# Kernel tuning notes

Hardware: AMD Instinct MI355X
Metric: run time of the kernel (lower is better)

The kernel has to match this reference:

```python
import jax, jax.numpy as jnp
import numpy as np

B = 2048
HID = 256      # hidden_dim (latent)
COND = 128     # cond_dim
NCH = 64       # n_chars
MAXLEN = 128   # max_len
R = 256        # recurrent_dim


def setup_inputs() -> dict:
    key = jax.random.key(0)
    ks = jax.random.split(key, 10)
    s = 0.05
    return {
        "z": jax.random.normal(ks[0], (B, HID), jnp.float32),
        "x_cond": jax.random.normal(ks[1], (B, COND), jnp.float32),
        # latent_to_hidden: Linear(hidden_dim + cond_dim -> recurrent_dim)
        "W_lh": jax.random.normal(ks[2], (R, HID + COND), jnp.float32) * s,
        "b_lh": jax.random.normal(ks[3], (R,), jnp.float32) * s,
        # GRU (single layer): weights in PyTorch gate order [r, z, n]
        "W_ih": jax.random.normal(ks[4], (3 * R, R), jnp.float32) * s,
        "W_hh": jax.random.normal(ks[5], (3 * R, R), jnp.float32) * s,
        "b_ih": jax.random.normal(ks[6], (3 * R,), jnp.float32) * s,
        "b_hh": jax.random.normal(ks[7], (3 * R,), jnp.float32) * s,
        # output_layer: Linear(recurrent_dim -> n_chars)
        "W_out": jax.random.normal(ks[8], (NCH, R), jnp.float32) * s,
        "b_out": jax.random.normal(ks[9], (NCH,), jnp.float32) * s,
    }


def _gru_cell(x, h, W_ih, W_hh, b_ih, b_hh):
    # PyTorch GRU cell: gates ordered [reset, update, new]
    gi = x @ W_ih.T + b_ih          # (B, 3R)
    gh = h @ W_hh.T + b_hh          # (B, 3R)
    i_r, i_z, i_n = jnp.split(gi, 3, axis=-1)
    h_r, h_z, h_n = jnp.split(gh, 3, axis=-1)
    r = jax.nn.sigmoid(i_r + h_r)
    u = jax.nn.sigmoid(i_z + h_z)
    n = jnp.tanh(i_n + r * h_n)
    return (1.0 - u) * n + u * h


def reference(z, x_cond, W_lh, b_lh, W_ih, W_hh, b_ih, b_hh, W_out, b_out):
    # Generation branch (teacher_force_inputs is None), dropout=0.0
    zc = jnp.concatenate([z, x_cond], axis=1)          # (B, HID+COND)
    h0 = zc @ W_lh.T + b_lh                            # (B, R), gru_depth=1
    x0 = jnp.zeros((z.shape[0], R), dtype=z.dtype)     # initial input step

    def step(carry, _):
        h, xin = carry
        hn = _gru_cell(xin, h, W_ih, W_hh, b_ih, b_hh)  # (B, R)
        logits = hn @ W_out.T + b_out                   # (B, NCH)
        return (hn, hn), logits                         # next input = GRU output

    (_, _), ys = jax.lax.scan(step, (h0, x0), None, length=MAXLEN)
    return jnp.transpose(ys, (1, 0, 2))                 # (B, MAXLEN, NCH)
```

## Files before the change

### kernel.cpp

```cpp
#include <hip/hip_runtime.h>
#include <hip/hip_bf16.h>

#define BATCH 2048
#define HID 256
#define COND 128
#define NCH 64
#define MAXLEN 128
#define RDIM 256

#define WCAT_OFF 0
#define WHH0_OFF 262144
#define WLH_OFF  524288
#define WOUT_OFF 622592
#define BCAT_OFF 638976
#define BCAT0_OFF 640000

__global__ void prep_kernel(const float* __restrict__ W_lh,
                            const float* __restrict__ W_ih, const float* __restrict__ W_hh,
                            const float* __restrict__ b_ih, const float* __restrict__ b_hh,
                            const float* __restrict__ W_out, float* __restrict__ ws) {
    int gid = blockIdx.x * blockDim.x + threadIdx.x;
    if (gid < 384 * 256) {
        int k = gid >> 8, u = gid & 255;
        ws[WLH_OFF + gid] = W_lh[u * 384 + k];
    }
    if (gid < 65536) {
        int k = gid >> 8, u = gid & 255;
        float ir = W_ih[u * 256 + k], iz = W_ih[(256 + u) * 256 + k], inw = W_ih[(512 + u) * 256 + k];
        float hr = W_hh[u * 256 + k], hz = W_hh[(256 + u) * 256 + k], hnw = W_hh[(512 + u) * 256 + k];
        int base = WCAT_OFF + k * 1024 + u * 4;
        ws[base + 0] = ir + hr; ws[base + 1] = iz + hz; ws[base + 2] = inw; ws[base + 3] = hnw;
        base = WHH0_OFF + k * 1024 + u * 4;
        ws[base + 0] = hr; ws[base + 1] = hz; ws[base + 2] = hnw; ws[base + 3] = 0.0f;
    }
    if (gid < 16384) {
        int k = gid >> 6, o = gid & 63;
        ws[WOUT_OFF + k * 64 + o] = W_out[o * 256 + k];
    }
    if (gid < 256) {
        int u = gid;
        float bir = b_ih[u], biz = b_ih[256 + u];
        float bhr = b_hh[u], bhz = b_hh[256 + u], bhn = b_hh[512 + u];
        int base = BCAT_OFF + u * 4;
        ws[base + 0] = bir + bhr; ws[base + 1] = biz + bhz; ws[base + 2] = b_ih[512 + u]; ws[base + 3] = bhn;
        base = BCAT0_OFF + u * 4;
        ws[base + 0] = bir + bhr; ws[base + 1] = biz + bhz; ws[base + 2] = bhn; ws[base + 3] = 0.0f;
    }
}

__device__ __forceinline__ float sigm(float x)   { return 1.0f / (1.0f + __expf(-x)); }
__device__ __forceinline__ float tanh_f(float x) { return 1.0f - 2.0f / (1.0f + __expf(2.0f * x)); }

__global__ __launch_bounds__(256)
void gru_persist(const float* __restrict__ z, const float* __restrict__ xc,
                 const float* __restrict__ b_lh, const float* __restrict__ b_ih,
                 const float* __restrict__ b_out_g,
                 const float* __restrict__ ws, float* __restrict__ out) {
    __shared__ __align__(16) float lds_h[8 * 256];
    __shared__ __align__(16) float lds_w[256 * 64];

    const int t  = threadIdx.x;
    const int b0 = blockIdx.x * 8;

    for (int idx = t; idx < 8 * 384; idx += 256) {
        int i = idx / 384, k = idx - i * 384;
        float v = (k < 256) ? z[(b0 + i) * 256 + k] : xc[(b0 + i) * 128 + (k - 256)];
        lds_w[i * 384 + k] = v;
    }
    __syncthreads();

    float h_own[8];
    {
        float acc[8];
        float blh = b_lh[t];
#pragma unroll
        for (int i = 0; i < 8; i++) acc[i] = blh;
        const float* Wlh = ws + WLH_OFF;
        for (int k4 = 0; k4 < 96; ++k4) {
            int k = k4 * 4;
            float w0 = Wlh[(k + 0) * 256 + t];
            float w1 = Wlh[(k + 1) * 256 + t];
            float w2 = Wlh[(k + 2) * 256 + t];
            float w3 = Wlh[(k + 3) * 256 + t];
#pragma unroll
            for (int i = 0; i < 8; i++) {
                const float4 hv = *(const float4*)&lds_w[i * 384 + k];
                acc[i] += hv.x * w0 + hv.y * w1 + hv.z * w2 + hv.w * w3;
            }
        }
#pragma unroll
        for (int i = 0; i < 8; i++) { h_own[i] = acc[i]; lds_h[i * 256 + t] = acc[i]; }
    }
    __syncthreads();

    {
        const float* Wo = ws + WOUT_OFF;
        for (int idx = t; idx < 16384; idx += 256) lds_w[idx] = Wo[idx];
    }
    __syncthreads();

    const float4* Wcat = (const float4*)(ws + WCAT_OFF);
    const float4* Whh0 = (const float4*)(ws + WHH0_OFF);
    const float4 bc1 = ((const float4*)(ws + BCAT_OFF))[t];
    const float4 bc0 = ((const float4*)(ws + BCAT0_OFF))[t];
    const float bin_c = b_ih[512 + t];
    const int olane = t & 63, rg = t >> 6;
    const float bout = b_out_g[olane];
    float* outp = out + (long)b0 * MAXLEN * NCH;

    for (int st = 0; st < MAXLEN; ++st) {
        const float4* Wp = (st == 0) ? Whh0 : Wcat;
        const float4 bc = (st == 0) ? bc0 : bc1;
        float ax[8], ay[8], az[8], aw[8];
#pragma unroll
        for (int i = 0; i < 8; i++) { ax[i] = bc.x; ay[i] = bc.y; az[i] = bc.z; aw[i] = bc.w; }

#pragma unroll 2
        for (int k4 = 0; k4 < 64; ++k4) {
            int k = k4 * 4;
            float4 w0 = Wp[(k + 0) * 256 + t];
            float4 w1 = Wp[(k + 1) * 256 + t];
            float4 w2 = Wp[(k + 2) * 256 + t];
            float4 w3 = Wp[(k + 3) * 256 + t];
#pragma unroll
            for (int i = 0; i < 8; i++) {
                const float4 hv = *(const float4*)&lds_h[i * 256 + k];
                ax[i] += hv.x * w0.x; ay[i] += hv.x * w0.y; az[i] += hv.x * w0.z; aw[i] += hv.x * w0.w;
                ax[i] += hv.y * w1.x; ay[i] += hv.y * w1.y; az[i] += hv.y * w1.z; aw[i] += hv.y * w1.w;
                ax[i] += hv.z * w2.x; ay[i] += hv.z * w2.y; az[i] += hv.z * w2.z; aw[i] += hv.z * w2.w;
                ax[i] += hv.w * w3.x; ay[i] += hv.w * w3.y; az[i] += hv.w * w3.z; aw[i] += hv.w * w3.w;
            }
        }

        float hn_[8];
        if (st == 0) {
#pragma unroll
            for (int i = 0; i < 8; i++) {
                float r = sigm(ax[i]); float uu = sigm(ay[i]);
                float n = tanh_f(bin_c + r * az[i]);
                hn_[i] = (1.0f - uu) * n + uu * h_own[i];
            }
        } else {
#pragma unroll
            for (int i = 0; i < 8; i++) {
                float r = sigm(ax[i]); float uu = sigm(ay[i]);
                float n = tanh_f(az[i] + r * aw[i]);
                hn_[i] = (1.0f - uu) * n + uu * h_own[i];
            }
        }
        __syncthreads();
#pragma unroll
        for (int i = 0; i < 8; i++) { lds_h[i * 256 + t] = hn_[i]; h_own[i] = hn_[i]; }
        __syncthreads();

        {
            float l0 = bout, l1 = bout;
            const int r0 = 2 * rg, r1 = 2 * rg + 1;
            for (int k4 = 0; k4 < 64; ++k4) {
                int k = k4 * 4;
                const float4 h0v = *(const float4*)&lds_h[r0 * 256 + k];
                const float4 h1v = *(const float4*)&lds_h[r1 * 256 + k];
                float wq0 = lds_w[(k + 0) * 64 + olane];
                float wq1 = lds_w[(k + 1) * 64 + olane];
                float wq2 = lds_w[(k + 2) * 64 + olane];
                float wq3 = lds_w[(k + 3) * 64 + olane];
                l0 += h0v.x * wq0 + h0v.y * wq1 + h0v.z * wq2 + h0v.w * wq3;
                l1 += h1v.x * wq0 + h1v.y * wq1 + h1v.z * wq2 + h1v.w * wq3;
            }
            outp[(long)r0 * MAXLEN * NCH + st * NCH + olane] = l0;
            outp[(long)r1 * MAXLEN * NCH + st * NCH + olane] = l1;
        }
    }
}

extern "C" void kernel_launch(void* const* d_in, const int* in_sizes, int n_in,
                              void* d_out, int out_size, void* d_ws, size_t ws_size,
                              hipStream_t stream) {
    const float* z     = (const float*)d_in[0];
    const float* xcond = (const float*)d_in[1];
    const float* W_lh  = (const float*)d_in[2];
    const float* b_lh  = (const float*)d_in[3];
    const float* W_ih  = (const float*)d_in[4];
    const float* W_hh  = (const float*)d_in[5];
    const float* b_ih  = (const float*)d_in[6];
    const float* b_hh  = (const float*)d_in[7];
    const float* W_out = (const float*)d_in[8];
    const float* b_out = (const float*)d_in[9];
    float* out = (float*)d_out;
    float* ws  = (float*)d_ws;

    hipLaunchKernelGGL(prep_kernel, dim3(384), dim3(256), 0, stream,
                       W_lh, W_ih, W_hh, b_ih, b_hh, W_out, ws);
    hipLaunchKernelGGL(gru_persist, dim3(256), dim3(256), 0, stream,
                       z, xcond, b_lh, b_ih, b_out, ws, out);
}
```

Measured before the change: 3.634 ms.

## Split GRU K-reduction across four wavegroups and overlap output projection with next step

Grows each block from 256 to 1024 threads. The 256-wide recurrent reduction is split four ways by K, with partial sums combined through LDS, so each thread's serial FMA chain per step is a quarter as long. The output-logit projection for the previous step now runs on the upper threads during the next step's reduction and reads W_out directly from global memory, so the LDS weight copy and its transpose in the prep kernel are dropped. The costs are extra LDS traffic and barriers for the partial-sum reduction, nonlinearities serialized on one quarter of the threads, and the launch bound of 1024 threads with 4 waves per EU may limit registers.

New measurement: 3.873 ms. +6.6%, slower.

```diff
diff --git a/kernel.cpp b/kernel.cpp
--- a/kernel.cpp
+++ b/kernel.cpp
@@ -11,14 +11,13 @@
 #define WCAT_OFF 0
 #define WHH0_OFF 262144
 #define WLH_OFF  524288
-#define WOUT_OFF 622592
 #define BCAT_OFF 638976
 #define BCAT0_OFF 640000
 
 __global__ void prep_kernel(const float* __restrict__ W_lh,
                             const float* __restrict__ W_ih, const float* __restrict__ W_hh,
                             const float* __restrict__ b_ih, const float* __restrict__ b_hh,
-                            const float* __restrict__ W_out, float* __restrict__ ws) {
+                            float* __restrict__ ws) {
     int gid = blockIdx.x * blockDim.x + threadIdx.x;
     if (gid < 384 * 256) {
         int k = gid >> 8, u = gid & 255;
@@ -33,10 +32,6 @@
         base = WHH0_OFF + k * 1024 + u * 4;
         ws[base + 0] = hr; ws[base + 1] = hz; ws[base + 2] = hnw; ws[base + 3] = 0.0f;
     }
-    if (gid < 16384) {
-        int k = gid >> 6, o = gid & 63;
-        ws[WOUT_OFF + k * 64 + o] = W_out[o * 256 + k];
-    }
     if (gid < 256) {
         int u = gid;
         float bir = b_ih[u], biz = b_ih[256 + u];
@@ -51,77 +46,83 @@
 __device__ __forceinline__ float sigm(float x)   { return 1.0f / (1.0f + __expf(-x)); }
 __device__ __forceinline__ float tanh_f(float x) { return 1.0f - 2.0f / (1.0f + __expf(2.0f * x)); }
 
-__global__ __launch_bounds__(256)
+__global__ __launch_bounds__(1024, 4)
 void gru_persist(const float* __restrict__ z, const float* __restrict__ xc,
                  const float* __restrict__ b_lh, const float* __restrict__ b_ih,
-                 const float* __restrict__ b_out_g,
+                 const float* __restrict__ W_out, const float* __restrict__ b_out_g,
                  const float* __restrict__ ws, float* __restrict__ out) {
     __shared__ __align__(16) float lds_h[8 * 256];
-    __shared__ __align__(16) float lds_w[256 * 64];
-
-    const int t  = threadIdx.x;
-    const int b0 = blockIdx.x * 8;
-
-    for (int idx = t; idx < 8 * 384; idx += 256) {
+    __shared__ __align__(16) float4 bufv[3 * 8 * 256];
+
+    const int tid = threadIdx.x;
+    const int u   = tid & 255;
+    const int q   = tid >> 8;
+    const int b0  = blockIdx.x * 8;
+
+    float* zcs = (float*)bufv;
+    for (int idx = tid; idx < 8 * 384; idx += 1024) {
         int i = idx / 384, k = idx - i * 384;
-        float v = (k < 256) ? z[(b0 + i) * 256 + k] : xc[(b0 + i) * 128 + (k - 256)];
-        lds_w[i * 384 + k] = v;
+        zcs[idx] = (k < 256) ? z[(b0 + i) * 256 + k] : xc[(b0 + i) * 128 + (k - 256)];
     }
     __syncthreads();
 
     float h_own[8];
-    {
+    if (q == 0) {
         float acc[8];
-        float blh = b_lh[t];
+        float blh = b_lh[u];
 #pragma unroll
         for (int i = 0; i < 8; i++) acc[i] = blh;
         const float* Wlh = ws + WLH_OFF;
         for (int k4 = 0; k4 < 96; ++k4) {
             int k = k4 * 4;
-            float w0 = Wlh[(k + 0) * 256 + t];
-            float w1 = Wlh[(k + 1) * 256 + t];
-            float w2 = Wlh[(k + 2) * 256 + t];
-            float w3 = Wlh[(k + 3) * 256 + t];
+            float w0 = Wlh[(k + 0) * 256 + u];
+            float w1 = Wlh[(k + 1) * 256 + u];
+            float w2 = Wlh[(k + 2) * 256 + u];
+            float w3 = Wlh[(k + 3) * 256 + u];
 #pragma unroll
             for (int i = 0; i < 8; i++) {
-                const float4 hv = *(const float4*)&lds_w[i * 384 + k];
+                const float4 hv = *(const float4*)&zcs[i * 384 + k];
                 acc[i] += hv.x * w0 + hv.y * w1 + hv.z * w2 + hv.w * w3;
             }
         }
 #pragma unroll
-        for (int i = 0; i < 8; i++) { h_own[i] = acc[i]; lds_h[i * 256 + t] = acc[i]; }
-    }
-    __syncthreads();
-
-    {
-        const float* Wo = ws + WOUT_OFF;
-        for (int idx = t; idx < 16384; idx += 256) lds_w[idx] = Wo[idx];
+        for (int i = 0; i < 8; i++) { h_own[i] = acc[i]; lds_h[i * 256 + u] = acc[i]; }
     }
     __syncthreads();
 
     const float4* Wcat = (const float4*)(ws + WCAT_OFF);
     const float4* Whh0 = (const float4*)(ws + WHH0_OFF);
-    const float4 bc1 = ((const float4*)(ws + BCAT_OFF))[t];
-    const float4 bc0 = ((const float4*)(ws + BCAT0_OFF))[t];
-    const float bin_c = b_ih[512 + t];
-    const int olane = t & 63, rg = t >> 6;
-    const float bout = b_out_g[olane];
+    const float4  bc1  = ((const float4*)(ws + BCAT_OFF))[u];
+    const float4  bc0  = ((const float4*)(ws + BCAT0_OFF))[u];
+    const float   bin_c = b_ih[512 + u];
+    const int kbase = q * 64;
+
+    const int lo_o = tid & 63;
+    const int lo_r = (tid - 512) >> 6;
+    const float bout = (tid >= 512) ? b_out_g[lo_o] : 0.0f;
+    const float4* Woutv = (const float4*)(W_out);
+    const float4* ldshv = (const float4*)lds_h;
     float* outp = out + (long)b0 * MAXLEN * NCH;
 
     for (int st = 0; st < MAXLEN; ++st) {
         const float4* Wp = (st == 0) ? Whh0 : Wcat;
-        const float4 bc = (st == 0) ? bc0 : bc1;
         float ax[8], ay[8], az[8], aw[8];
-#pragma unroll
-        for (int i = 0; i < 8; i++) { ax[i] = bc.x; ay[i] = bc.y; az[i] = bc.z; aw[i] = bc.w; }
+        if (q == 0) {
+            const float4 bc = (st == 0) ? bc0 : bc1;
+#pragma unroll
+            for (int i = 0; i < 8; i++) { ax[i] = bc.x; ay[i] = bc.y; az[i] = bc.z; aw[i] = bc.w; }
+        } else {
+#pragma unroll
+            for (int i = 0; i < 8; i++) { ax[i] = 0.0f; ay[i] = 0.0f; az[i] = 0.0f; aw[i] = 0.0f; }
+        }
 
 #pragma unroll 2
-        for (int k4 = 0; k4 < 64; ++k4) {
-            int k = k4 * 4;
-            float4 w0 = Wp[(k + 0) * 256 + t];
-            float4 w1 = Wp[(k + 1) * 256 + t];
-            float4 w2 = Wp[(k + 2) * 256 + t];
-            float4 w3 = Wp[(k + 3) * 256 + t];
+        for (int k4 = 0; k4 < 16; ++k4) {
+            int k = kbase + k4 * 4;
+            float4 w0 = Wp[(k + 0) * 256 + u];
+            float4 w1 = Wp[(k + 1) * 256 + u];
+            float4 w2 = Wp[(k + 2) * 256 + u];
+            float4 w3 = Wp[(k + 3) * 256 + u];
 #pragma unroll
             for (int i = 0; i < 8; i++) {
                 const float4 hv = *(const float4*)&lds_h[i * 256 + k];
@@ -132,44 +133,64 @@
             }
         }
 
-        float hn_[8];
-        if (st == 0) {
-#pragma unroll
-            for (int i = 0; i < 8; i++) {
-                float r = sigm(ax[i]); float uu = sigm(ay[i]);
-                float n = tanh_f(bin_c + r * az[i]);
-                hn_[i] = (1.0f - uu) * n + uu * h_own[i];
-            }
-        } else {
-#pragma unroll
-            for (int i = 0; i < 8; i++) {
-                float r = sigm(ax[i]); float uu = sigm(ay[i]);
-                float n = tanh_f(az[i] + r * aw[i]);
-                hn_[i] = (1.0f - uu) * n + uu * h_own[i];
-            }
-        }
+        if (q) {
+#pragma unroll
+            for (int i = 0; i < 8; i++)
+                bufv[(q - 1) * 2048 + i * 256 + u] = make_float4(ax[i], ay[i], az[i], aw[i]);
+        }
+
+        if (tid >= 512 && st > 0) {
+            float l = bout;
+#pragma unroll 4
+            for (int k4 = 0; k4 < 64; ++k4) {
+                const float4 w = Woutv[lo_o * 64 + k4];
+                const float4 h = ldshv[lo_r * 64 + k4];
+                l += h.x * w.x + h.y * w.y + h.z * w.z + h.w * w.w;
+            }
+            outp[(long)lo_r * MAXLEN * NCH + (st - 1) * NCH + lo_o] = l;
+        }
+
         __syncthreads();
-#pragma unroll
-        for (int i = 0; i < 8; i++) { lds_h[i * 256 + t] = hn_[i]; h_own[i] = hn_[i]; }
+
+        if (q == 0) {
+#pragma unroll
+            for (int qq = 0; qq < 3; ++qq)
+#pragma unroll
+                for (int i = 0; i < 8; ++i) {
+                    const float4 p = bufv[qq * 2048 + i * 256 + u];
+                    ax[i] += p.x; ay[i] += p.y; az[i] += p.z; aw[i] += p.w;
+                }
+            float hn_[8];
+            if (st == 0) {
+#pragma unroll
+                for (int i = 0; i < 8; i++) {
+                    float r = sigm(ax[i]); float uu = sigm(ay[i]);
+                    float n = tanh_f(bin_c + r * az[i]);
+                    hn_[i] = (1.0f - uu) * n + uu * h_own[i];
+                }
+            } else {
+#pragma unroll
+                for (int i = 0; i < 8; i++) {
+                    float r = sigm(ax[i]); float uu = sigm(ay[i]);
+                    float n = tanh_f(az[i] + r * aw[i]);
+                    hn_[i] = (1.0f - uu) * n + uu * h_own[i];
+                }
+            }
+#pragma unroll
+            for (int i = 0; i < 8; i++) { lds_h[i * 256 + u] = hn_[i]; h_own[i] = hn_[i]; }
+        }
         __syncthreads();
-
-        {
-            float l0 = bout, l1 = bout;
-            const int r0 = 2 * rg, r1 = 2 * rg + 1;
-            for (int k4 = 0; k4 < 64; ++k4) {
-                int k = k4 * 4;
-                const float4 h0v = *(const float4*)&lds_h[r0 * 256 + k];
-                const float4 h1v = *(const float4*)&lds_h[r1 * 256 + k];
-                float wq0 = lds_w[(k + 0) * 64 + olane];
-                float wq1 = lds_w[(k + 1) * 64 + olane];
-                float wq2 = lds_w[(k + 2) * 64 + olane];
-                float wq3 = lds_w[(k + 3) * 64 + olane];
-                l0 += h0v.x * wq0 + h0v.y * wq1 + h0v.z * wq2 + h0v.w * wq3;
-                l1 += h1v.x * wq0 + h1v.y * wq1 + h1v.z * wq2 + h1v.w * wq3;
-            }
-            outp[(long)r0 * MAXLEN * NCH + st * NCH + olane] = l0;
-            outp[(long)r1 * MAXLEN * NCH + st * NCH + olane] = l1;
-        }
+    }
+
+    if (tid >= 512) {
+        float l = bout;
+#pragma unroll 4
+        for (int k4 = 0; k4 < 64; ++k4) {
+            const float4 w = Woutv[lo_o * 64 + k4];
+            const float4 h = ldshv[lo_r * 64 + k4];
+            l += h.x * w.x + h.y * w.y + h.z * w.z + h.w * w.w;
+        }
+        outp[(long)lo_r * MAXLEN * NCH + (MAXLEN - 1) * NCH + lo_o] = l;
     }
 }
 
@@ -190,7 +211,7 @@
     float* ws  = (float*)d_ws;
 
     hipLaunchKernelGGL(prep_kernel, dim3(384), dim3(256), 0, stream,
-                       W_lh, W_ih, W_hh, b_ih, b_hh, W_out, ws);
-    hipLaunchKernelGGL(gru_persist, dim3(256), dim3(256), 0, stream,
-                       z, xcond, b_lh, b_ih, b_out, ws, out);
+                       W_lh, W_ih, W_hh, b_ih, b_hh, ws);
+    hipLaunchKernelGGL(gru_persist, dim3(256), dim3(1024), 0, stream,
+                       z, xcond, b_lh, b_ih, W_out, b_out, ws, out);
 }
```

## Split GRU K-reduction across four wavegroups with LDS partial-sum exchange

Applied to the files above, without the earlier changes.

The block grows from 256 to 1024 threads: each quarter of threads computes a partial matvec over a 64-wide slice of the hidden dimension for all 8 rows, then writes the partials to LDS. Each thread then reduces the partials for two rows and applies the gate math. The output projection is deferred by one step, reads W_out from global memory instead of LDS, and is split in two halves reduced through LDS. The goal is more parallelism per CU on the serial recurrence. In exchange the kernel uses more LDS, adds a partial-sum exchange every step, and repeatedly streams W_out from global/L2.

Result: faster. 3.333 ms (-8.3%).

```diff
diff --git a/kernel.cpp b/kernel.cpp
--- a/kernel.cpp
+++ b/kernel.cpp
@@ -2,8 +2,6 @@
 #include <hip/hip_bf16.h>
 
 #define BATCH 2048
-#define HID 256
-#define COND 128
 #define NCH 64
 #define MAXLEN 128
 #define RDIM 256
@@ -34,7 +32,7 @@
         ws[base + 0] = hr; ws[base + 1] = hz; ws[base + 2] = hnw; ws[base + 3] = 0.0f;
     }
     if (gid < 16384) {
-        int k = gid >> 6, o = gid & 63;
+        int o = gid & 63, k = gid >> 6;
         ws[WOUT_OFF + k * 64 + o] = W_out[o * 256 + k];
     }
     if (gid < 256) {
@@ -51,125 +49,156 @@
 __device__ __forceinline__ float sigm(float x)   { return 1.0f / (1.0f + __expf(-x)); }
 __device__ __forceinline__ float tanh_f(float x) { return 1.0f - 2.0f / (1.0f + __expf(2.0f * x)); }
 
-__global__ __launch_bounds__(256)
+__global__ __launch_bounds__(1024, 1)
 void gru_persist(const float* __restrict__ z, const float* __restrict__ xc,
                  const float* __restrict__ b_lh, const float* __restrict__ b_ih,
                  const float* __restrict__ b_out_g,
                  const float* __restrict__ ws, float* __restrict__ out) {
     __shared__ __align__(16) float lds_h[8 * 256];
-    __shared__ __align__(16) float lds_w[256 * 64];
-
-    const int t  = threadIdx.x;
-    const int b0 = blockIdx.x * 8;
-
-    for (int idx = t; idx < 8 * 384; idx += 256) {
+    __shared__ __align__(16) float4 pbufv[4 * 6 * 256];
+    __shared__ float lbuf[1024];
+
+    const int tid = threadIdx.x;
+    const int u   = tid & 255;
+    const int q   = __builtin_amdgcn_readfirstlane(tid >> 8);
+    const int b0  = blockIdx.x * 8;
+
+    float* zcs = (float*)pbufv;
+    for (int idx = tid; idx < 8 * 384; idx += 1024) {
         int i = idx / 384, k = idx - i * 384;
-        float v = (k < 256) ? z[(b0 + i) * 256 + k] : xc[(b0 + i) * 128 + (k - 256)];
-        lds_w[i * 384 + k] = v;
+        zcs[idx] = (k < 256) ? z[(b0 + i) * 256 + k] : xc[(b0 + i) * 128 + (k - 256)];
     }
     __syncthreads();
 
-    float h_own[8];
+    float h_own0, h_own1;
     {
-        float acc[8];
-        float blh = b_lh[t];
-#pragma unroll
-        for (int i = 0; i < 8; i++) acc[i] = blh;
-        const float* Wlh = ws + WLH_OFF;
+        float a0 = b_lh[u], a1 = a0;
+        const float* Wlh = ws + WLH_OFF + u;
+        const float* zr0 = zcs + (2 * q) * 384;
+        const float* zr1 = zr0 + 384;
+#pragma unroll 2
         for (int k4 = 0; k4 < 96; ++k4) {
-            int k = k4 * 4;
-            float w0 = Wlh[(k + 0) * 256 + t];
-            float w1 = Wlh[(k + 1) * 256 + t];
-            float w2 = Wlh[(k + 2) * 256 + t];
-            float w3 = Wlh[(k + 3) * 256 + t];
-#pragma unroll
-            for (int i = 0; i < 8; i++) {
-                const float4 hv = *(const float4*)&lds_w[i * 384 + k];
-                acc[i] += hv.x * w0 + hv.y * w1 + hv.z * w2 + hv.w * w3;
+            int k = 4 * k4;
+            float w0 = Wlh[(k + 0) * 256];
+            float w1 = Wlh[(k + 1) * 256];
+            float w2 = Wlh[(k + 2) * 256];
+            float w3 = Wlh[(k + 3) * 256];
+            const float4 v0 = *(const float4*)(zr0 + k);
+            const float4 v1 = *(const float4*)(zr1 + k);
+            a0 += v0.x * w0 + v0.y * w1 + v0.z * w2 + v0.w * w3;
+            a1 += v1.x * w0 + v1.y * w1 + v1.z * w2 + v1.w * w3;
+        }
+        h_own0 = a0; h_own1 = a1;
+        lds_h[(2 * q) * 256 + u] = a0;
+        lds_h[(2 * q + 1) * 256 + u] = a1;
+    }
+    __syncthreads();
+
+    const float4* Wcat  = (const float4*)(ws + WCAT_OFF);
+    const float4* Whh0v = (const float4*)(ws + WHH0_OFF);
+    const float4  bc1   = ((const float4*)(ws + BCAT_OFF))[u];
+    const float4  bc0v  = ((const float4*)(ws + BCAT0_OFF))[u];
+    const float   bin_c = b_ih[512 + u];
+
+    int ro[8];
+#pragma unroll
+    for (int jj = 0; jj < 8; ++jj) ro[jj] = (((2 * q + jj) & 7) << 8);
+
+    const int lkh = tid & 1;
+    const float* hrow_base = lds_h + ((tid >> 1) >> 6) * 256 + lkh * 128;
+    const float* wcolT = ws + WOUT_OFF + lkh * 128 * 64 + ((tid >> 1) & 63);
+    const int co = tid & 63, cr = tid >> 6;
+    const float bout = b_out_g[co];
+    float* outp = out + (long)b0 * MAXLEN * NCH;
+
+    for (int st = 0; st < MAXLEN; ++st) {
+        const float4* Wp = st ? Wcat : Whh0v;
+        float ax[8], ay[8], az[8], aw[8];
+#pragma unroll
+        for (int jj = 0; jj < 8; ++jj) { ax[jj] = 0.f; ay[jj] = 0.f; az[jj] = 0.f; aw[jj] = 0.f; }
+
+        const float4* wbase = Wp + (q * 64) * 256 + u;
+        const float*  hbase = lds_h + q * 64;
+
+#pragma unroll 2
+        for (int k4 = 0; k4 < 16; ++k4) {
+            const float4 w0 = wbase[(4 * k4 + 0) * 256];
+            const float4 w1 = wbase[(4 * k4 + 1) * 256];
+            const float4 w2 = wbase[(4 * k4 + 2) * 256];
+            const float4 w3 = wbase[(4 * k4 + 3) * 256];
+#pragma unroll
+            for (int jj = 0; jj < 8; ++jj) {
+                const float4 hv = *(const float4*)(hbase + ro[jj] + 4 * k4);
+                ax[jj] += hv.x * w0.x; ay[jj] += hv.x * w0.y; az[jj] += hv.x * w0.z; aw[jj] += hv.x * w0.w;
+                ax[jj] += hv.y * w1.x; ay[jj] += hv.y * w1.y; az[jj] += hv.y * w1.z; aw[jj] += hv.y * w1.w;
+                ax[jj] += hv.z * w2.x; ay[jj] += hv.z * w2.y; az[jj] += hv.z * w2.z; aw[jj] += hv.z * w2.w;
+                ax[jj] += hv.w * w3.x; ay[jj] += hv.w * w3.y; az[jj] += hv.w * w3.z; aw[jj] += hv.w * w3.w;
             }
         }
-#pragma unroll
-        for (int i = 0; i < 8; i++) { h_own[i] = acc[i]; lds_h[i * 256 + t] = acc[i]; }
+
+        {
+            float4* pb = pbufv + q * 6 * 256 + u;
+#pragma unroll
+            for (int j = 0; j < 6; ++j)
+                pb[j * 256] = make_float4(ax[j + 2], ay[j + 2], az[j + 2], aw[j + 2]);
+        }
+
+        if (st) {
+            float l = 0.f;
+#pragma unroll 8
+            for (int kk = 0; kk < 128; ++kk) l += hrow_base[kk] * wcolT[kk * 64];
+            lbuf[tid] = l;
+        }
+
+        __syncthreads();
+
+#pragma unroll
+        for (int qq = 0; qq < 4; ++qq) {
+            if (qq != q) {
+                const int j0 = (2 * q - 2 * qq - 2) & 7;
+                const float4 p0 = pbufv[(qq * 6 + j0) * 256 + u];
+                const float4 p1 = pbufv[(qq * 6 + j0 + 1) * 256 + u];
+                ax[0] += p0.x; ay[0] += p0.y; az[0] += p0.z; aw[0] += p0.w;
+                ax[1] += p1.x; ay[1] += p1.y; az[1] += p1.z; aw[1] += p1.w;
+            }
+        }
+        float hn0, hn1;
+        if (st == 0) {
+            float r0 = sigm(ax[0] + bc0v.x), z0 = sigm(ay[0] + bc0v.y);
+            float n0 = tanh_f(bin_c + r0 * (az[0] + bc0v.z));
+            hn0 = (1.f - z0) * n0 + z0 * h_own0;
+            float r1 = sigm(ax[1] + bc0v.x), z1 = sigm(ay[1] + bc0v.y);
+            float n1 = tanh_f(bin_c + r1 * (az[1] + bc0v.z));
+            hn1 = (1.f - z1) * n1 + z1 * h_own1;
+        } else {
+            float r0 = sigm(ax[0] + bc1.x), z0 = sigm(ay[0] + bc1.y);
+            float n0 = tanh_f(az[0] + bc1.z + r0 * (aw[0] + bc1.w));
+            hn0 = (1.f - z0) * n0 + z0 * h_own0;
+            float r1 = sigm(ax[1] + bc1.x), z1 = sigm(ay[1] + bc1.y);
+            float n1 = tanh_f(az[1] + bc1.z + r1 * (aw[1] + bc1.w));
+            hn1 = (1.f - z1) * n1 + z1 * h_own1;
+        }
+        lds_h[(2 * q) * 256 + u] = hn0;
+        lds_h[(2 * q + 1) * 256 + u] = hn1;
+        h_own0 = hn0; h_own1 = hn1;
+
+        if (st && tid < 512) {
+            float l = lbuf[2 * tid] + lbuf[2 * tid + 1] + bout;
+            outp[(long)cr * MAXLEN * NCH + (st - 1) * NCH + co] = l;
+        }
+        __syncthreads();
+    }
+
+    {
+        float l = 0.f;
+#pragma unroll 8
+        for (int kk = 0; kk < 128; ++kk) l += hrow_base[kk] * wcolT[kk * 64];
+        lbuf[tid] = l;
     }
     __syncthreads();
-
-    {
-        const float* Wo = ws + WOUT_OFF;
-        for (int idx = t; idx < 16384; idx += 256) lds_w[idx] = Wo[idx];
-    }
-    __syncthreads();
-
-    const float4* Wcat = (const float4*)(ws + WCAT_OFF);
-    const float4* Whh0 = (const float4*)(ws + WHH0_OFF);
-    const float4 bc1 = ((const float4*)(ws + BCAT_OFF))[t];
-    const float4 bc0 = ((const float4*)(ws + BCAT0_OFF))[t];
-    const float bin_c = b_ih[512 + t];
-    const int olane = t & 63, rg = t >> 6;
-    const float bout = b_out_g[olane];
-    float* outp = out + (long)b0 * MAXLEN * NCH;
-
-    for (int st = 0; st < MAXLEN; ++st) {
-        const float4* Wp = (st == 0) ? Whh0 : Wcat;
-        const float4 bc = (st == 0) ? bc0 : bc1;
-        float ax[8], ay[8], az[8], aw[8];
-#pragma unroll
-        for (int i = 0; i < 8; i++) { ax[i] = bc.x; ay[i] = bc.y; az[i] = bc.z; aw[i] = bc.w; }
-
-#pragma unroll 2
-        for (int k4 = 0; k4 < 64; ++k4) {
-            int k = k4 * 4;
-            float4 w0 = Wp[(k + 0) * 256 + t];
-            float4 w1 = Wp[(k + 1) * 256 + t];
-            float4 w2 = Wp[(k + 2) * 256 + t];
-            float4 w3 = Wp[(k + 3) * 256 + t];
-#pragma unroll
-            for (int i = 0; i < 8; i++) {
-                const float4 hv = *(const float4*)&lds_h[i * 256 + k];
-                ax[i] += hv.x * w0.x; ay[i] += hv.x * w0.y; az[i] += hv.x * w0.z; aw[i] += hv.x * w0.w;
-                ax[i] += hv.y * w1.x; ay[i] += hv.y * w1.y; az[i] += hv.y * w1.z; aw[i] += hv.y * w1.w;
-                ax[i] += hv.z * w2.x; ay[i] += hv.z * w2.y; az[i] += hv.z * w2.z; aw[i] += hv.z * w2.w;
-                ax[i] += hv.w * w3.x; ay[i] += hv.w * w3.y; az[i] += hv.w * w3.z; aw[i] += hv.w * w3.w;
-            }
-        }
-
-        float hn_[8];
-        if (st == 0) {
-#pragma unroll
-            for (int i = 0; i < 8; i++) {
-                float r = sigm(ax[i]); float uu = sigm(ay[i]);
-                float n = tanh_f(bin_c + r * az[i]);
-                hn_[i] = (1.0f - uu) * n + uu * h_own[i];
-            }
-        } else {
-#pragma unroll
-            for (int i = 0; i < 8; i++) {
-                float r = sigm(ax[i]); float uu = sigm(ay[i]);
-                float n = tanh_f(az[i] + r * aw[i]);
-                hn_[i] = (1.0f - uu) * n + uu * h_own[i];
-            }
-        }
-        __syncthreads();
-#pragma unroll
-        for (int i = 0; i < 8; i++) { lds_h[i * 256 + t] = hn_[i]; h_own[i] = hn_[i]; }
-        __syncthreads();
-
-        {
-            float l0 = bout, l1 = bout;
-            const int r0 = 2 * rg, r1 = 2 * rg + 1;
-            for (int k4 = 0; k4 < 64; ++k4) {
-                int k = k4 * 4;
-                const float4 h0v = *(const float4*)&lds_h[r0 * 256 + k];
-                const float4 h1v = *(const float4*)&lds_h[r1 * 256 + k];
-                float wq0 = lds_w[(k + 0) * 64 + olane];
-                float wq1 = lds_w[(k + 1) * 64 + olane];
-                float wq2 = lds_w[(k + 2) * 64 + olane];
-                float wq3 = lds_w[(k + 3) * 64 + olane];
-                l0 += h0v.x * wq0 + h0v.y * wq1 + h0v.z * wq2 + h0v.w * wq3;
-                l1 += h1v.x * wq0 + h1v.y * wq1 + h1v.z * wq2 + h1v.w * wq3;
-            }
-            outp[(long)r0 * MAXLEN * NCH + st * NCH + olane] = l0;
-            outp[(long)r1 * MAXLEN * NCH + st * NCH + olane] = l1;
-        }
+    if (tid < 512) {
+        float l = lbuf[2 * tid] + lbuf[2 * tid + 1] + bout;
+        outp[(long)cr * MAXLEN * NCH + (MAXLEN - 1) * NCH + co] = l;
     }
 }
 
@@ -191,6 +220,6 @@
 
     hipLaunchKernelGGL(prep_kernel, dim3(384), dim3(256), 0, stream,
                        W_lh, W_ih, W_hh, b_ih, b_hh, W_out, ws);
-    hipLaunchKernelGGL(gru_persist, dim3(256), dim3(256), 0, stream,
+    hipLaunchKernelGGL(gru_persist, dim3(256), dim3(1024), 0, stream,
                        z, xcond, b_lh, b_ih, b_out, ws, out);
 }
```
